# Kernel optimization log

Measured on AMD Instinct MI355X. Metric: run time of the kernel, lower is better.

## Reference

```python
import jax, jax.numpy as jnp
import numpy as np

EPS = 1e-5
NUM_PIXELS = 2  # M_Relax window half-width


def _conv(x, w, b, groups=1, pad=0):
    y = jax.lax.conv_general_dilated(
        x, w, (1, 1), [(pad, pad), (pad, pad)],
        dimension_numbers=("NCHW", "OIHW", "NCHW"),
        feature_group_count=groups)
    return y + b[None, :, None, None]


def _bn(x, g, bta, m, v):
    # eval-mode BatchNorm2d with running stats
    inv = jax.lax.rsqrt(v + EPS)
    return g[None, :, None, None] * (x - m[None, :, None, None]) * inv[None, :, None, None] + bta[None, :, None, None]


def _resb(x, w1, b1, w2, b2):
    y = _conv(x, w1, b1, groups=4, pad=1)
    y = jnp.where(y > 0, y, 0.1 * y)  # LeakyReLU(0.1)
    y = _conv(y, w2, b2, groups=4, pad=1)
    return y + x


def _relax(M):
    # M: (N, w, w); sum of shifts +-NUM_PIXELS along the row (dim 1)
    w = M.shape[1]
    P = jnp.pad(M, ((0, 0), (NUM_PIXELS, NUM_PIXELS), (0, 0)))
    out = P[:, 0:w, :]
    for k in range(1, 2 * NUM_PIXELS + 1):
        out = out + P[:, k:k + w, :]
    return out


def setup_inputs() -> dict:
    key = jax.random.key(0)
    ks = jax.random.split(key, 16)
    b, c, h, w = 4, 64, 128, 256
    c2 = 2 * c
    s = 0.05
    inp = {
        "x_left": jax.random.normal(ks[0], (b, c, h, w), jnp.float32),
        "x_right": jax.random.normal(ks[1], (b, c, h, w), jnp.float32),
        "conv1_w": jax.random.normal(ks[2], (c, c, 1, 1), jnp.float32) * s,
        "conv1_b": jnp.zeros((c,), jnp.float32),
        "conv2_w": jax.random.normal(ks[3], (c, c, 1, 1), jnp.float32) * s,
        "conv2_b": jnp.zeros((c,), jnp.float32),
        "bn_g": jnp.ones((c2,), jnp.float32),
        "bn_b": jnp.zeros((c2,), jnp.float32),
        "bn_m": jax.random.normal(ks[4], (c2,), jnp.float32) * 0.1,
        "bn_v": jax.random.uniform(ks[5], (c2,), jnp.float32) + 0.5,
        "rb_w1": jax.random.normal(ks[6], (c2, c2 // 4, 3, 3), jnp.float32) * s,
        "rb_b1": jnp.zeros((c2,), jnp.float32),
        "rb_w2": jax.random.normal(ks[7], (c2, c2 // 4, 3, 3), jnp.float32) * s,
        "rb_b2": jnp.zeros((c2,), jnp.float32),
        "bq_w": jax.random.normal(ks[8], (c, c, 1, 1), jnp.float32) * s,
        "bq_b": jnp.zeros((c,), jnp.float32),
        "bs_w": jax.random.normal(ks[9], (c, c, 1, 1), jnp.float32) * s,
        "bs_b": jnp.zeros((c,), jnp.float32),
    }
    return inp


def reference(x_left, x_right, conv1_w, conv1_b, conv2_w, conv2_b,
              bn_g, bn_b, bn_m, bn_v, rb_w1, rb_b1, rb_w2, rb_b2,
              bq_w, bq_b, bs_w, bs_b):
    b, c, h, w = x_left.shape
    cat_l = jnp.concatenate([_conv(x_left, conv1_w, conv1_b), x_left], axis=1)
    cat_r = jnp.concatenate([_conv(x_right, conv2_w, conv2_b), x_right], axis=1)
    Q = _conv(_resb(_bn(cat_l, bn_g, bn_b, bn_m, bn_v), rb_w1, rb_b1, rb_w2, rb_b2), bq_w, bq_b, groups=2)
    K = _conv(_resb(_bn(cat_r, bn_g, bn_b, bn_m, bn_v), rb_w1, rb_b1, rb_w2, rb_b2), bs_w, bs_b, groups=2)
    Q = Q - Q.mean(axis=3, keepdims=True)
    K = K - K.mean(axis=3, keepdims=True)
    # score: (b*h, w, w) -- per-epipolar-row cross-view attention
    Qr = Q.transpose(0, 2, 3, 1).reshape(b * h, w, c)
    Kr = K.transpose(0, 2, 1, 3).reshape(b * h, c, w)
    score = jnp.matmul(Qr, Kr)
    M_r2l = jax.nn.softmax(score, axis=-1)
    M_l2r = jax.nn.softmax(score.transpose(0, 2, 1), axis=-1)
    # validity maps via relaxed cycle-consistency (detached in original)
    V_l = jnp.einsum("nij,nji->ni", _relax(M_r2l), M_l2r)
    V_r = jnp.einsum("nij,nji->ni", _relax(M_l2r), M_r2l)
    V_l = jax.lax.stop_gradient(V_l).reshape(b, 1, h, w)
    V_r = jax.lax.stop_gradient(V_r).reshape(b, 1, h, w)
    V_l_t = jnp.tanh(5.0 * V_l)
    V_r_t = jnp.tanh(5.0 * V_r)
    xl = x_left.transpose(0, 2, 3, 1).reshape(b * h, w, c)
    xr = x_right.transpose(0, 2, 3, 1).reshape(b * h, w, c)
    x_lT = jnp.matmul(M_r2l, xr).reshape(b, h, w, c).transpose(0, 3, 1, 2)
    x_rT = jnp.matmul(M_l2r, xl).reshape(b, h, w, c).transpose(0, 3, 1, 2)
    out_left = x_left * (1.0 - V_l_t) + x_lT * V_l_t
    out_right = x_right * (1.0 - V_r_t) + x_rT * V_r_t
    return out_left, out_right
```

## Files before the change

### kernel.cpp

```cpp
#include <hip/hip_runtime.h>
#include <math.h>

#define BB 4
#define CC 64
#define C2 128
#define HH 128
#define WW 256
#define NN (BB*HH)
#define EPSBN 1e-5f

typedef _Float16 f16;
typedef _Float16 half8 __attribute__((ext_vector_type(8)));
typedef float f32x4 __attribute__((ext_vector_type(4)));

__global__ __launch_bounds__(256) void k_wprep(
    const float* __restrict__ w1, const float* __restrict__ w2,
    f16* __restrict__ wp1, f16* __restrict__ wp2)
{
    int g = blockIdx.x; int which = blockIdx.y;
    const float* src = which ? w2 : w1;
    f16* dst = which ? wp2 : wp1;
    for (int p = threadIdx.x; p < 9216; p += 256) {
        int mo = p / 288; int kr = p - mo*288;
        int ks = kr >> 5; int ic = kr & 31;
        dst[g*9216 + p] = (f16)src[((g*32 + mo)*32 + ic)*9 + ks];
    }
}

__global__ __launch_bounds__(256) void k_catbn_m(
    const float* __restrict__ x, const float* __restrict__ cw, const float* __restrict__ cb,
    const float* __restrict__ g, const float* __restrict__ bb_, const float* __restrict__ m,
    const float* __restrict__ v, f16* __restrict__ u)
{
    __shared__ f16 Xl[256][72];
    __shared__ f16 Wl[64][72];
    __shared__ float sS[64], sT[64], sS2[64], sT2[64];
    int n = blockIdx.x; int b = n >> 7; int h = n & 127; int t = threadIdx.x;
    for (int p = t; p < 2048; p += 256) {
        int idx = p * 2; int o = idx >> 6, i = idx & 63;
        union { f16 h[2]; unsigned int u1; } pr;
        pr.h[0] = (f16)cw[idx]; pr.h[1] = (f16)cw[idx + 1];
        *(unsigned int*)&Wl[o][i] = pr.u1;
    }
    if (t < 64) {
        float inv = rsqrtf(v[t] + EPSBN); float s = g[t] * inv;
        sS[t] = s; sT[t] = bb_[t] + s * (cb[t] - m[t]);
        float inv2 = rsqrtf(v[t + 64] + EPSBN); float s2 = g[t + 64] * inv2;
        sS2[t] = s2; sT2[t] = bb_[t + 64] - s2 * m[t + 64];
    }
    __syncthreads();
    f16* up = u + ((size_t)(n*256 + t)) * 128;
    for (int c8 = 0; c8 < 8; ++c8) {
        float xv8[8];
#pragma unroll
        for (int j = 0; j < 8; ++j)
            xv8[j] = x[(((b*64 + c8*8 + j)*128 + h) << 8) + t];
        union { f16 h[8]; uint4 v4; } pk;
#pragma unroll
        for (int j = 0; j < 8; ++j) {
            int c = c8*8 + j;
            pk.h[j] = (f16)(sS2[c]*xv8[j] + sT2[c]);
        }
        *(uint4*)(up + 64 + c8*8) = pk.v4;
#pragma unroll
        for (int j2 = 0; j2 < 4; ++j2) {
            union { f16 h[2]; unsigned int u1; } q;
            q.h[0] = (f16)xv8[j2*2]; q.h[1] = (f16)xv8[j2*2 + 1];
            *(unsigned int*)&Xl[t][c8*8 + j2*2] = q.u1;
        }
    }
    __syncthreads();
    int lane = t & 63, wv = t >> 6;
    int m16 = lane & 15, quad = lane >> 4;
    half8 af[4][2], bf[4][2];
#pragma unroll
    for (int mt = 0; mt < 4; ++mt)
#pragma unroll
        for (int kk = 0; kk < 2; ++kk)
            af[mt][kk] = *(const half8*)&Wl[mt*16 + m16][kk*32 + quad*8];
#pragma unroll
    for (int nt = 0; nt < 4; ++nt)
#pragma unroll
        for (int kk = 0; kk < 2; ++kk)
            bf[nt][kk] = *(const half8*)&Xl[wv*64 + nt*16 + m16][kk*32 + quad*8];
    f32x4 acc[4][4] = {};
#pragma unroll
    for (int mt = 0; mt < 4; ++mt)
#pragma unroll
        for (int nt = 0; nt < 4; ++nt) {
            acc[mt][nt] = __builtin_amdgcn_mfma_f32_16x16x32_f16(af[mt][0], bf[nt][0], acc[mt][nt], 0, 0, 0);
            acc[mt][nt] = __builtin_amdgcn_mfma_f32_16x16x32_f16(af[mt][1], bf[nt][1], acc[mt][nt], 0, 0, 0);
        }
#pragma unroll
    for (int mt = 0; mt < 4; ++mt) {
        int ocb = mt*16 + quad*4;
        float s4[4], t4[4];
        *(float4*)s4 = *(const float4*)&sS[ocb];
        *(float4*)t4 = *(const float4*)&sT[ocb];
#pragma unroll
        for (int nt = 0; nt < 4; ++nt) {
            int px = wv*64 + nt*16 + m16;
            union { f16 h[4]; uint2 u2; } ov;
#pragma unroll
            for (int r = 0; r < 4; ++r)
                ov.h[r] = (f16)(s4[r]*acc[mt][nt][r] + t4[r]);
            *(uint2*)(u + ((size_t)(n*256 + px))*128 + ocb) = ov.u2;
        }
    }
}

template<bool LEAKY, bool RES>
__global__ __launch_bounds__(256, 2) void k_conv3r(
    const f16* __restrict__ in, const f16* __restrict__ wp,
    const float* __restrict__ bias, const f16* __restrict__ res,
    f16* __restrict__ out)
{
    __shared__ f16 Xl[6*130*40];
    int b = blockIdx.x >> 5; int h0 = (blockIdx.x & 31) * 4;
    int g = blockIdx.y; int w0 = blockIdx.z * 128;
    int t = threadIdx.x;
    int lane = t & 63, wv = t >> 6;
    int m16 = lane & 15, quad = lane >> 4;
    const f16* wg = wp + g*9216;
    half8 af[2][9];
#pragma unroll
    for (int mt = 0; mt < 2; ++mt)
#pragma unroll
        for (int ks = 0; ks < 9; ++ks)
            af[mt][ks] = *(const half8*)(wg + (mt*16 + m16)*288 + ks*32 + quad*8);
    float bo[2][4];
#pragma unroll
    for (int mt = 0; mt < 2; ++mt)
#pragma unroll
        for (int r = 0; r < 4; ++r)
            bo[mt][r] = bias[g*32 + mt*16 + quad*4 + r];
    for (int idx = t; idx < 3120; idx += 256) {
        int r = idx / 520; int rem = idx - r*520; int p = rem >> 2; int q = rem & 3;
        int hr = h0 + r - 1; int wg2 = w0 + p - 1;
        uint4 val = make_uint4(0,0,0,0);
        if ((unsigned)wg2 < 256u && (unsigned)hr < 128u)
            val = *(const uint4*)(in + ((size_t)((b*128 + hr)*256 + wg2))*128 + g*32 + q*8);
        *(uint4*)&Xl[(r*130 + p)*40 + q*8] = val;
    }
    __syncthreads();
    int px0 = wv*32 + m16;
#pragma unroll
    for (int rr = 0; rr < 4; ++rr) {
        f32x4 acc[2][2] = {};
#pragma unroll
        for (int ks = 0; ks < 9; ++ks) {
            int ky = ks / 3, kx = ks - ky*3;
            half8 bf0 = *(const half8*)&Xl[((rr + ky)*130 + px0 + kx)*40 + quad*8];
            half8 bf1 = *(const half8*)&Xl[((rr + ky)*130 + px0 + 16 + kx)*40 + quad*8];
            acc[0][0] = __builtin_amdgcn_mfma_f32_16x16x32_f16(af[0][ks], bf0, acc[0][0], 0, 0, 0);
            acc[0][1] = __builtin_amdgcn_mfma_f32_16x16x32_f16(af[0][ks], bf1, acc[0][1], 0, 0, 0);
            acc[1][0] = __builtin_amdgcn_mfma_f32_16x16x32_f16(af[1][ks], bf0, acc[1][0], 0, 0, 0);
            acc[1][1] = __builtin_amdgcn_mfma_f32_16x16x32_f16(af[1][ks], bf1, acc[1][1], 0, 0, 0);
        }
        int h = h0 + rr;
#pragma unroll
        for (int mt = 0; mt < 2; ++mt)
#pragma unroll
            for (int nt = 0; nt < 2; ++nt) {
                int px = w0 + wv*32 + nt*16 + m16;
                int oc = g*32 + mt*16 + quad*4;
                size_t off = ((size_t)((b*128 + h)*256 + px))*128 + oc;
                float rv4[4] = {0.f, 0.f, 0.f, 0.f};
                if (RES) {
                    union { f16 h[4]; uint2 v2; } rrd;
                    rrd.v2 = *(const uint2*)(res + off);
#pragma unroll
                    for (int r = 0; r < 4; ++r) rv4[r] = (float)rrd.h[r];
                }
                union { f16 h[4]; uint2 v2; } ov;
#pragma unroll
                for (int r = 0; r < 4; ++r) {
                    float y = acc[mt][nt][r] + bo[mt][r];
                    if (LEAKY) y = y > 0.f ? y : 0.1f*y;
                    if (RES) y += rv4[r];
                    ov.h[r] = (f16)y;
                }
                *(uint2*)(out + off) = ov.v2;
            }
    }
}

__global__ __launch_bounds__(256, 2) void k_conv1x1m(
    const f16* __restrict__ in, const float* __restrict__ wgt,
    f16* __restrict__ outq)
{
    __shared__ f16 Xl[256][72];
    __shared__ f16 Wl[64][72];
    __shared__ float partial[4][64];
    __shared__ float meanS[64];
    int n = blockIdx.x; int t = threadIdx.x;
    int lane = t & 63, wv = t >> 6;
    int m16 = lane & 15, quad = lane >> 4;
    for (int p = t; p < 2048; p += 256) {
        int idx = p * 2; int o = idx >> 6, i = idx & 63;
        union { f16 h[2]; unsigned int u1; } pr;
        pr.h[0] = (f16)wgt[idx]; pr.h[1] = (f16)wgt[idx + 1];
        *(unsigned int*)&Wl[o][i] = pr.u1;
    }
    f32x4 acc[4][4] = {};
    const f16* rp = in + ((size_t)n*256 + t)*128;
    for (int g = 0; g < 2; ++g) {
#pragma unroll
        for (int i8 = 0; i8 < 8; ++i8)
            *(uint4*)&Xl[t][i8*8] = *(const uint4*)(rp + g*64 + i8*8);
        __syncthreads();
        half8 af[2][2], bf[4][2];
#pragma unroll
        for (int ml = 0; ml < 2; ++ml)
#pragma unroll
            for (int kk = 0; kk < 2; ++kk)
                af[ml][kk] = *(const half8*)&Wl[g*32 + ml*16 + m16][kk*32 + quad*8];
#pragma unroll
        for (int nt = 0; nt < 4; ++nt)
#pragma unroll
            for (int kk = 0; kk < 2; ++kk)
                bf[nt][kk] = *(const half8*)&Xl[wv*64 + nt*16 + m16][kk*32 + quad*8];
#pragma unroll
        for (int ml = 0; ml < 2; ++ml)
#pragma unroll
            for (int nt = 0; nt < 4; ++nt) {
                int mt = g*2 + ml;
                acc[mt][nt] = __builtin_amdgcn_mfma_f32_16x16x32_f16(af[ml][0], bf[nt][0], acc[mt][nt], 0, 0, 0);
                acc[mt][nt] = __builtin_amdgcn_mfma_f32_16x16x32_f16(af[ml][1], bf[nt][1], acc[mt][nt], 0, 0, 0);
            }
        __syncthreads();
    }
#pragma unroll
    for (int mt = 0; mt < 4; ++mt)
#pragma unroll
        for (int r = 0; r < 4; ++r) {
            float s = acc[mt][0][r] + acc[mt][1][r] + acc[mt][2][r] + acc[mt][3][r];
            s += __shfl_xor(s, 1); s += __shfl_xor(s, 2);
            s += __shfl_xor(s, 4); s += __shfl_xor(s, 8);
            if (m16 == 0) partial[wv][mt*16 + quad*4 + r] = s;
        }
    __syncthreads();
    if (t < 64)
        meanS[t] = (partial[0][t] + partial[1][t] + partial[2][t] + partial[3][t]) * (1.0f/256.0f);
    __syncthreads();
    f16* qp = outq + ((size_t)n*256)*64;
#pragma unroll
    for (int mt = 0; mt < 4; ++mt) {
        int ocb = mt*16 + quad*4;
        float m4[4]; *(float4*)m4 = *(const float4*)&meanS[ocb];
#pragma unroll
        for (int nt = 0; nt < 4; ++nt) {
            int px = wv*64 + nt*16 + m16;
            union { f16 h[4]; uint2 u2; } ov;
#pragma unroll
            for (int r = 0; r < 4; ++r)
                ov.h[r] = (f16)(acc[mt][nt][r] - m4[r]);
            *(uint2*)(qp + (size_t)px*64 + ocb) = ov.u2;
        }
    }
}

__global__ __launch_bounds__(512, 1) void k_attn(
    const f16* __restrict__ Aq, const f16* __restrict__ Bk,
    const float* __restrict__ xB, const float* __restrict__ xP,
    float* __restrict__ outp)
{
    __shared__ f16 Sl[65536];
    __shared__ f16 Pl[260][40];
    __shared__ f16 Xl[64][40];
    __shared__ float rmS[256], riS[256], cmS[256], ciS[256];
    __shared__ float scr[2][256];
    int n = blockIdx.x; int b = n >> 7; int h = n & 127;
    int t = threadIdx.x;
    int lane = t & 63, wv = t >> 6;
    int m16 = lane & 15, quad = lane >> 4;
    int W = wv * 32;

    const f16* ag = Aq + (size_t)n*16384;
    const f16* bg = Bk + (size_t)n*16384;
    half8 af1[2][2];
#pragma unroll
    for (int mt = 0; mt < 2; ++mt)
#pragma unroll
        for (int kk = 0; kk < 2; ++kk)
            af1[mt][kk] = *(const half8*)(ag + (size_t)(W + mt*16 + m16)*64 + kk*32 + quad*8);
    for (int jc = 0; jc < 256; jc += 64) {
        half8 bf1[4][2];
#pragma unroll
        for (int nt = 0; nt < 4; ++nt)
#pragma unroll
            for (int kk = 0; kk < 2; ++kk)
                bf1[nt][kk] = *(const half8*)(bg + (size_t)(jc + nt*16 + m16)*64 + kk*32 + quad*8);
        f32x4 acc1[2][4] = {};
#pragma unroll
        for (int mt = 0; mt < 2; ++mt)
#pragma unroll
            for (int nt = 0; nt < 4; ++nt) {
                acc1[mt][nt] = __builtin_amdgcn_mfma_f32_16x16x32_f16(af1[mt][0], bf1[nt][0], acc1[mt][nt], 0, 0, 0);
                acc1[mt][nt] = __builtin_amdgcn_mfma_f32_16x16x32_f16(af1[mt][1], bf1[nt][1], acc1[mt][nt], 0, 0, 0);
            }
#pragma unroll
        for (int mt = 0; mt < 2; ++mt)
#pragma unroll
            for (int nt = 0; nt < 4; ++nt)
#pragma unroll
                for (int r = 0; r < 4; ++r) {
                    int row = W + mt*16 + quad*4 + r;
                    int col = jc + nt*16 + m16;
                    int byte = (row << 9) + ((col*2) ^ ((row & 7) << 4));
                    *(f16*)((char*)Sl + byte) = (f16)acc1[mt][nt][r];
                }
    }
    __syncthreads();

    if (t < 256) {
        int r = t; int xo = (r & 7) << 4;
        const char* base = (const char*)Sl + (r << 9);
        float m = -1e30f;
#pragma unroll 4
        for (int g = 0; g < 32; ++g) {
            half8 v8 = *(const half8*)(base + ((g*16) ^ xo));
#pragma unroll
            for (int e = 0; e < 8; ++e) m = fmaxf(m, (float)v8[e]);
        }
        float s = 0.f;
#pragma unroll 4
        for (int g = 0; g < 32; ++g) {
            half8 v8 = *(const half8*)(base + ((g*16) ^ xo));
#pragma unroll
            for (int e = 0; e < 8; ++e) s += __expf((float)v8[e] - m);
        }
        rmS[r] = m; riS[r] = 1.0f/s;
    } else {
        int c = t - 256; int c2 = c*2;
        const char* base = (const char*)Sl;
        float m = -1e30f;
#pragma unroll 8
        for (int row = 0; row < 256; ++row) {
            f16 v = *(const f16*)(base + (row << 9) + (c2 ^ ((row & 7) << 4)));
            m = fmaxf(m, (float)v);
        }
        float s = 0.f;
#pragma unroll 8
        for (int row = 0; row < 256; ++row) {
            f16 v = *(const f16*)(base + (row << 9) + (c2 ^ ((row & 7) << 4)));
            s += __expf((float)v - m);
        }
        cmS[c] = m; ciS[c] = 1.0f/s;
    }
    if (t < 10)       *(uint4*)((char*)&Pl[0][0]   + t*16)      = make_uint4(0,0,0,0);
    else if (t < 20)  *(uint4*)((char*)&Pl[258][0] + (t-10)*16) = make_uint4(0,0,0,0);
    __syncthreads();

    int r = t & 255, hc = t >> 8;
    int cbase = hc * 16;
    float rm = rmS[r], ri = riS[r];
    int xc = t >> 3, xj = (t & 7) * 4;
    const float* xg = xB + ((size_t)(b*64 + xc)*128 + h)*256;
    f32x4 acc[2][4] = {};
    float vacc = 0.f;
    const char* sb = (const char*)Sl + (r << 9);
    int xo = (r & 7) << 4;
    for (int kc = 0; kc < 256; kc += 32) {
        float sraw[16];
        {
            half8 v0 = *(const half8*)(sb + ((((kc + cbase)*2))      ^ xo));
            half8 v1 = *(const half8*)(sb + ((((kc + cbase)*2) + 16) ^ xo));
            half8 p0, p1;
#pragma unroll
            for (int e = 0; e < 8; ++e) {
                sraw[e] = (float)v0[e];
                p0[e] = (f16)(__expf(sraw[e] - rm) * ri);
            }
#pragma unroll
            for (int e = 0; e < 8; ++e) {
                sraw[8 + e] = (float)v1[e];
                p1[e] = (f16)(__expf(sraw[8 + e] - rm) * ri);
            }
            char* pb = (char*)&Pl[r + 2][cbase];
            *(half8*)pb = p0; *(half8*)(pb + 16) = p1;
        }
        {
            float4 x4 = *(const float4*)(xg + kc + xj);
            union { f16 h[4]; uint2 v2; } px;
            px.h[0] = (f16)x4.x; px.h[1] = (f16)x4.y;
            px.h[2] = (f16)x4.z; px.h[3] = (f16)x4.w;
            *(uint2*)&Xl[xc][xj] = px.v2;
        }
        __syncthreads();
#pragma unroll
        for (int j8 = 0; j8 < 2; ++j8) {
            const char* wb = (const char*)&Pl[r][cbase + j8*8];
            half8 w0 = *(const half8*)(wb);
            half8 w1 = *(const half8*)(wb + 80);
            half8 w2 = *(const half8*)(wb + 160);
            half8 w3 = *(const half8*)(wb + 240);
            half8 w4 = *(const half8*)(wb + 320);
            half8 win = w0 + w1 + w2 + w3 + w4;
#pragma unroll
            for (int e = 0; e < 8; ++e) {
                int j = kc + cbase + j8*8 + e;
                float Bv = __expf(sraw[j8*8 + e] - cmS[j]) * ciS[j];
                vacc = fmaf((float)win[e], Bv, vacc);
            }
        }
        half8 pa[2], xb_[4];
#pragma unroll
        for (int mt = 0; mt < 2; ++mt)
            pa[mt] = *(const half8*)((const char*)&Pl[W + mt*16 + m16 + 2][0] + quad*16);
#pragma unroll
        for (int nt = 0; nt < 4; ++nt)
            xb_[nt] = *(const half8*)((const char*)&Xl[nt*16 + m16][0] + quad*16);
#pragma unroll
        for (int mt = 0; mt < 2; ++mt)
#pragma unroll
            for (int nt = 0; nt < 4; ++nt)
                acc[mt][nt] = __builtin_amdgcn_mfma_f32_16x16x32_f16(pa[mt], xb_[nt], acc[mt][nt], 0, 0, 0);
        __syncthreads();
    }
    scr[hc][r] = vacc;
    __syncthreads();
    if (t < 256) rmS[t] = scr[0][t] + scr[1][t];
    __syncthreads();
#pragma unroll
    for (int mt = 0; mt < 2; ++mt) {
        int i0 = W + mt*16 + quad*4;
        float v4[4];
        *(float4*)v4 = *(const float4*)&rmS[i0];
        float tv[4];
#pragma unroll
        for (int rr = 0; rr < 4; ++rr) tv[rr] = tanhf(5.f*v4[rr]);
#pragma unroll
        for (int nt = 0; nt < 4; ++nt) {
            int c = nt*16 + m16;
            size_t base = (((size_t)(b*64 + c)*128 + h) << 8) + i0;
            float xp4[4]; *(float4*)xp4 = *(const float4*)&xP[base];
            float o4[4];
#pragma unroll
            for (int rr = 0; rr < 4; ++rr)
                o4[rr] = xp4[rr]*(1.f - tv[rr]) + acc[mt][nt][rr]*tv[rr];
            *(float4*)&outp[base] = *(float4*)o4;
        }
    }
}

extern "C" void kernel_launch(void* const* d_in, const int* in_sizes, int n_in,
                              void* d_out, int out_size, void* d_ws, size_t ws_size,
                              hipStream_t stream)
{
    const float* x_left  = (const float*)d_in[0];
    const float* x_right = (const float*)d_in[1];
    const float* conv1_w = (const float*)d_in[2];
    const float* conv1_b = (const float*)d_in[3];
    const float* conv2_w = (const float*)d_in[4];
    const float* conv2_b = (const float*)d_in[5];
    const float* bn_g    = (const float*)d_in[6];
    const float* bn_b    = (const float*)d_in[7];
    const float* bn_m    = (const float*)d_in[8];
    const float* bn_v    = (const float*)d_in[9];
    const float* rb_w1   = (const float*)d_in[10];
    const float* rb_b1   = (const float*)d_in[11];
    const float* rb_w2   = (const float*)d_in[12];
    const float* rb_b2   = (const float*)d_in[13];
    const float* bq_w    = (const float*)d_in[14];
    const float* bs_w    = (const float*)d_in[16];

    f16* W16 = (f16*)d_ws;
    f16* u  = W16;
    f16* y1 = W16 + 16777216;
    f16* r  = W16 + 33554432;
    f16* Qh = W16 + 67108864;
    f16* Kh = W16 + 75497472;
    f16* Wp1 = W16 + 84934656;
    f16* Wp2 = W16 + 84971520;

    float* out_left  = (float*)d_out;
    float* out_right = (float*)d_out + 8388608;

    k_wprep<<<dim3(4, 2), 256, 0, stream>>>(rb_w1, rb_w2, Wp1, Wp2);

    k_catbn_m<<<NN, 256, 0, stream>>>(x_left, conv1_w, conv1_b, bn_g, bn_b, bn_m, bn_v, u);
    k_conv3r<true,  false><<<dim3(128, 4, 2), 256, 0, stream>>>(u, Wp1, rb_b1, nullptr, y1);
    k_conv3r<false, true ><<<dim3(128, 4, 2), 256, 0, stream>>>(y1, Wp2, rb_b2, u, r);
    k_conv1x1m<<<NN, 256, 0, stream>>>(r, bq_w, Qh);

    k_catbn_m<<<NN, 256, 0, stream>>>(x_right, conv2_w, conv2_b, bn_g, bn_b, bn_m, bn_v, u);
    k_conv3r<true,  false><<<dim3(128, 4, 2), 256, 0, stream>>>(u, Wp1, rb_b1, nullptr, y1);
    k_conv3r<false, true ><<<dim3(128, 4, 2), 256, 0, stream>>>(y1, Wp2, rb_b2, u, r);
    k_conv1x1m<<<NN, 256, 0, stream>>>(r, bs_w, Kh);

    k_attn<<<NN, 512, 0, stream>>>(Qh, Kh, x_right, x_left,  out_left);
    k_attn<<<NN, 512, 0, stream>>>(Kh, Qh, x_left,  x_right, out_right);
}
```

Measured before the change: 520.6 us.

## Fuse both attention directions into one kernel sharing score matrix and online softmax stats

Merges the two k_attn launches into a single kernel that computes the Q·K score tile once and reuses it transposed for the right-to-left pass. Row and column softmax max/sum are computed online from MFMA registers with wave shuffles instead of separate scans over shared memory. This removes a duplicate score GEMM and the serial column-reduction loop. The cost is strided transposed reads from shared memory in the second pass and more register pressure.

```diff
diff --git a/kernel.cpp b/kernel.cpp
--- a/kernel.cpp
+++ b/kernel.cpp
@@ -260,123 +260,51 @@
     }
 }
 
-__global__ __launch_bounds__(512, 1) void k_attn(
-    const f16* __restrict__ Aq, const f16* __restrict__ Bk,
+
+template<int RIGHT>
+__device__ __forceinline__ void attn_pass(
+    const char* Sl, char* pool,
+    const float* __restrict__ myM, const float* __restrict__ myI,
+    const float* __restrict__ oM,  const float* __restrict__ oI,
     const float* __restrict__ xB, const float* __restrict__ xP,
-    float* __restrict__ outp)
-{
-    __shared__ f16 Sl[65536];
-    __shared__ f16 Pl[260][40];
-    __shared__ f16 Xl[64][40];
-    __shared__ float rmS[256], riS[256], cmS[256], ciS[256];
-    __shared__ float scr[2][256];
-    int n = blockIdx.x; int b = n >> 7; int h = n & 127;
-    int t = threadIdx.x;
+    float* __restrict__ outp, int b, int h, int t)
+{
+    f16 (*Pl)[40] = (f16(*)[40])pool;
+    f16 (*Xl)[40] = (f16(*)[40])(pool + 20800);
+    float* scr = (float*)(pool + 20800);
+    float* Vv  = (float*)(pool + 22848);
     int lane = t & 63, wv = t >> 6;
     int m16 = lane & 15, quad = lane >> 4;
     int W = wv * 32;
-
-    const f16* ag = Aq + (size_t)n*16384;
-    const f16* bg = Bk + (size_t)n*16384;
-    half8 af1[2][2];
-#pragma unroll
-    for (int mt = 0; mt < 2; ++mt)
-#pragma unroll
-        for (int kk = 0; kk < 2; ++kk)
-            af1[mt][kk] = *(const half8*)(ag + (size_t)(W + mt*16 + m16)*64 + kk*32 + quad*8);
-    for (int jc = 0; jc < 256; jc += 64) {
-        half8 bf1[4][2];
-#pragma unroll
-        for (int nt = 0; nt < 4; ++nt)
-#pragma unroll
-            for (int kk = 0; kk < 2; ++kk)
-                bf1[nt][kk] = *(const half8*)(bg + (size_t)(jc + nt*16 + m16)*64 + kk*32 + quad*8);
-        f32x4 acc1[2][4] = {};
-#pragma unroll
-        for (int mt = 0; mt < 2; ++mt)
-#pragma unroll
-            for (int nt = 0; nt < 4; ++nt) {
-                acc1[mt][nt] = __builtin_amdgcn_mfma_f32_16x16x32_f16(af1[mt][0], bf1[nt][0], acc1[mt][nt], 0, 0, 0);
-                acc1[mt][nt] = __builtin_amdgcn_mfma_f32_16x16x32_f16(af1[mt][1], bf1[nt][1], acc1[mt][nt], 0, 0, 0);
-            }
-#pragma unroll
-        for (int mt = 0; mt < 2; ++mt)
-#pragma unroll
-            for (int nt = 0; nt < 4; ++nt)
-#pragma unroll
-                for (int r = 0; r < 4; ++r) {
-                    int row = W + mt*16 + quad*4 + r;
-                    int col = jc + nt*16 + m16;
-                    int byte = (row << 9) + ((col*2) ^ ((row & 7) << 4));
-                    *(f16*)((char*)Sl + byte) = (f16)acc1[mt][nt][r];
-                }
-    }
-    __syncthreads();
-
-    if (t < 256) {
-        int r = t; int xo = (r & 7) << 4;
-        const char* base = (const char*)Sl + (r << 9);
-        float m = -1e30f;
-#pragma unroll 4
-        for (int g = 0; g < 32; ++g) {
-            half8 v8 = *(const half8*)(base + ((g*16) ^ xo));
-#pragma unroll
-            for (int e = 0; e < 8; ++e) m = fmaxf(m, (float)v8[e]);
-        }
-        float s = 0.f;
-#pragma unroll 4
-        for (int g = 0; g < 32; ++g) {
-            half8 v8 = *(const half8*)(base + ((g*16) ^ xo));
-#pragma unroll
-            for (int e = 0; e < 8; ++e) s += __expf((float)v8[e] - m);
-        }
-        rmS[r] = m; riS[r] = 1.0f/s;
-    } else {
-        int c = t - 256; int c2 = c*2;
-        const char* base = (const char*)Sl;
-        float m = -1e30f;
-#pragma unroll 8
-        for (int row = 0; row < 256; ++row) {
-            f16 v = *(const f16*)(base + (row << 9) + (c2 ^ ((row & 7) << 4)));
-            m = fmaxf(m, (float)v);
-        }
-        float s = 0.f;
-#pragma unroll 8
-        for (int row = 0; row < 256; ++row) {
-            f16 v = *(const f16*)(base + (row << 9) + (c2 ^ ((row & 7) << 4)));
-            s += __expf((float)v - m);
-        }
-        cmS[c] = m; ciS[c] = 1.0f/s;
-    }
-    if (t < 10)       *(uint4*)((char*)&Pl[0][0]   + t*16)      = make_uint4(0,0,0,0);
-    else if (t < 20)  *(uint4*)((char*)&Pl[258][0] + (t-10)*16) = make_uint4(0,0,0,0);
-    __syncthreads();
-
     int r = t & 255, hc = t >> 8;
     int cbase = hc * 16;
-    float rm = rmS[r], ri = riS[r];
+    float rm = myM[r], ri = myI[r];
     int xc = t >> 3, xj = (t & 7) * 4;
     const float* xg = xB + ((size_t)(b*64 + xc)*128 + h)*256;
     f32x4 acc[2][4] = {};
     float vacc = 0.f;
-    const char* sb = (const char*)Sl + (r << 9);
+    const char* sb = Sl + (r << 9);
     int xo = (r & 7) << 4;
     for (int kc = 0; kc < 256; kc += 32) {
         float sraw[16];
+        if (!RIGHT) {
+            half8 v0 = *(const half8*)(sb + (((kc + cbase)*2)      ^ xo));
+            half8 v1 = *(const half8*)(sb + (((kc + cbase)*2 + 16) ^ xo));
+#pragma unroll
+            for (int e = 0; e < 8; ++e) { sraw[e] = (float)v0[e]; sraw[8+e] = (float)v1[e]; }
+        } else {
+#pragma unroll
+            for (int e = 0; e < 16; ++e) {
+                int j = kc + cbase + e;
+                sraw[e] = (float)*(const f16*)(Sl + (j << 9) + ((r*2) ^ ((j & 7) << 4)));
+            }
+        }
         {
-            half8 v0 = *(const half8*)(sb + ((((kc + cbase)*2))      ^ xo));
-            half8 v1 = *(const half8*)(sb + ((((kc + cbase)*2) + 16) ^ xo));
             half8 p0, p1;
 #pragma unroll
-            for (int e = 0; e < 8; ++e) {
-                sraw[e] = (float)v0[e];
-                p0[e] = (f16)(__expf(sraw[e] - rm) * ri);
-            }
-#pragma unroll
-            for (int e = 0; e < 8; ++e) {
-                sraw[8 + e] = (float)v1[e];
-                p1[e] = (f16)(__expf(sraw[8 + e] - rm) * ri);
-            }
+            for (int e = 0; e < 8; ++e) p0[e] = (f16)(__expf(sraw[e]     - rm) * ri);
+#pragma unroll
+            for (int e = 0; e < 8; ++e) p1[e] = (f16)(__expf(sraw[8 + e] - rm) * ri);
             char* pb = (char*)&Pl[r + 2][cbase];
             *(half8*)pb = p0; *(half8*)(pb + 16) = p1;
         }
@@ -400,7 +328,7 @@
 #pragma unroll
             for (int e = 0; e < 8; ++e) {
                 int j = kc + cbase + j8*8 + e;
-                float Bv = __expf(sraw[j8*8 + e] - cmS[j]) * ciS[j];
+                float Bv = __expf(sraw[j8*8 + e] - oM[j]) * oI[j];
                 vacc = fmaf((float)win[e], Bv, vacc);
             }
         }
@@ -418,15 +346,15 @@
                 acc[mt][nt] = __builtin_amdgcn_mfma_f32_16x16x32_f16(pa[mt], xb_[nt], acc[mt][nt], 0, 0, 0);
         __syncthreads();
     }
-    scr[hc][r] = vacc;
-    __syncthreads();
-    if (t < 256) rmS[t] = scr[0][t] + scr[1][t];
+    scr[hc*256 + r] = vacc;
+    __syncthreads();
+    if (t < 256) Vv[t] = scr[t] + scr[256 + t];
     __syncthreads();
 #pragma unroll
     for (int mt = 0; mt < 2; ++mt) {
         int i0 = W + mt*16 + quad*4;
         float v4[4];
-        *(float4*)v4 = *(const float4*)&rmS[i0];
+        *(float4*)v4 = *(const float4*)&Vv[i0];
         float tv[4];
 #pragma unroll
         for (int rr = 0; rr < 4; ++rr) tv[rr] = tanhf(5.f*v4[rr]);
@@ -442,6 +370,132 @@
             *(float4*)&outp[base] = *(float4*)o4;
         }
     }
+}
+
+__global__ __launch_bounds__(512, 1) void k_attn2(
+    const f16* __restrict__ Q, const f16* __restrict__ K,
+    const float* __restrict__ xl, const float* __restrict__ xr,
+    float* __restrict__ outL, float* __restrict__ outR)
+{
+    __shared__ f16 Sl[65536];
+    __shared__ __align__(16) char pool[25920];
+    __shared__ float rmS[256], riS[256], cmS[256], ciS[256];
+    float* colM = (float*)pool;
+    float* colS = (float*)(pool + 8192);
+    int n = blockIdx.x; int b = n >> 7; int h = n & 127;
+    int t = threadIdx.x;
+    int lane = t & 63, wv = t >> 6;
+    int m16 = lane & 15, quad = lane >> 4;
+    int W = wv * 32;
+
+    const f16* ag = Q + (size_t)n*16384;
+    const f16* bg = K + (size_t)n*16384;
+    half8 af1[2][2];
+#pragma unroll
+    for (int mt = 0; mt < 2; ++mt)
+#pragma unroll
+        for (int kk = 0; kk < 2; ++kk)
+            af1[mt][kk] = *(const half8*)(ag + (size_t)(W + mt*16 + m16)*64 + kk*32 + quad*8);
+    float rowm[8], rows_[8];
+#pragma unroll
+    for (int i = 0; i < 8; ++i) { rowm[i] = -1e30f; rows_[i] = 0.f; }
+    for (int jc = 0; jc < 256; jc += 64) {
+        half8 bf1[4][2];
+#pragma unroll
+        for (int nt = 0; nt < 4; ++nt)
+#pragma unroll
+            for (int kk = 0; kk < 2; ++kk)
+                bf1[nt][kk] = *(const half8*)(bg + (size_t)(jc + nt*16 + m16)*64 + kk*32 + quad*8);
+        f32x4 acc1[2][4] = {};
+#pragma unroll
+        for (int mt = 0; mt < 2; ++mt)
+#pragma unroll
+            for (int nt = 0; nt < 4; ++nt) {
+                acc1[mt][nt] = __builtin_amdgcn_mfma_f32_16x16x32_f16(af1[mt][0], bf1[nt][0], acc1[mt][nt], 0, 0, 0);
+                acc1[mt][nt] = __builtin_amdgcn_mfma_f32_16x16x32_f16(af1[mt][1], bf1[nt][1], acc1[mt][nt], 0, 0, 0);
+            }
+#pragma unroll
+        for (int mt = 0; mt < 2; ++mt)
+#pragma unroll
+            for (int nt = 0; nt < 4; ++nt)
+#pragma unroll
+                for (int r = 0; r < 4; ++r) {
+                    int row = W + mt*16 + quad*4 + r;
+                    int col = jc + nt*16 + m16;
+                    f16 hv = (f16)acc1[mt][nt][r];
+                    *(f16*)((char*)Sl + (row << 9) + ((col*2) ^ ((row & 7) << 4))) = hv;
+                    acc1[mt][nt][r] = (float)hv;
+                }
+#pragma unroll
+        for (int mt = 0; mt < 2; ++mt)
+#pragma unroll
+            for (int r = 0; r < 4; ++r) {
+                float lm = fmaxf(fmaxf(acc1[mt][0][r], acc1[mt][1][r]),
+                                 fmaxf(acc1[mt][2][r], acc1[mt][3][r]));
+                lm = fmaxf(lm, __shfl_xor(lm, 1));
+                lm = fmaxf(lm, __shfl_xor(lm, 2));
+                lm = fmaxf(lm, __shfl_xor(lm, 4));
+                lm = fmaxf(lm, __shfl_xor(lm, 8));
+                float le = __expf(acc1[mt][0][r] - lm) + __expf(acc1[mt][1][r] - lm)
+                         + __expf(acc1[mt][2][r] - lm) + __expf(acc1[mt][3][r] - lm);
+                le += __shfl_xor(le, 1); le += __shfl_xor(le, 2);
+                le += __shfl_xor(le, 4); le += __shfl_xor(le, 8);
+                int idx = mt*4 + r;
+                float nm = fmaxf(rowm[idx], lm);
+                rows_[idx] = rows_[idx]*__expf(rowm[idx] - nm) + le*__expf(lm - nm);
+                rowm[idx] = nm;
+            }
+#pragma unroll
+        for (int nt = 0; nt < 4; ++nt) {
+            float lm = acc1[0][nt][0];
+#pragma unroll
+            for (int r = 1; r < 4; ++r) lm = fmaxf(lm, acc1[0][nt][r]);
+#pragma unroll
+            for (int r = 0; r < 4; ++r) lm = fmaxf(lm, acc1[1][nt][r]);
+            lm = fmaxf(lm, __shfl_xor(lm, 16));
+            lm = fmaxf(lm, __shfl_xor(lm, 32));
+            float le = 0.f;
+#pragma unroll
+            for (int mt2 = 0; mt2 < 2; ++mt2)
+#pragma unroll
+                for (int r = 0; r < 4; ++r) le += __expf(acc1[mt2][nt][r] - lm);
+            le += __shfl_xor(le, 16); le += __shfl_xor(le, 32);
+            if (quad == 0) {
+                int col = jc + nt*16 + m16;
+                colM[wv*256 + col] = lm;
+                colS[wv*256 + col] = le;
+            }
+        }
+    }
+    if (m16 == 0) {
+#pragma unroll
+        for (int mt = 0; mt < 2; ++mt)
+#pragma unroll
+            for (int r = 0; r < 4; ++r) {
+                int row = W + mt*16 + quad*4 + r;
+                rmS[row] = rowm[mt*4 + r];
+                riS[row] = 1.0f / rows_[mt*4 + r];
+            }
+    }
+    __syncthreads();
+    if (t < 256) {
+        float m = colM[t], s = colS[t];
+#pragma unroll
+        for (int w = 1; w < 8; ++w) {
+            float m2 = colM[w*256 + t], s2 = colS[w*256 + t];
+            float nm = fmaxf(m, m2);
+            s = s*__expf(m - nm) + s2*__expf(m2 - nm);
+            m = nm;
+        }
+        cmS[t] = m; ciS[t] = 1.0f / s;
+    }
+    __syncthreads();
+    if (t < 10)       *(uint4*)(pool + t*16)           = make_uint4(0,0,0,0);
+    else if (t < 20)  *(uint4*)(pool + 20640 + (t-10)*16) = make_uint4(0,0,0,0);
+
+    attn_pass<0>((const char*)Sl, pool, rmS, riS, cmS, ciS, xr, xl, outL, b, h, t);
+    __syncthreads();
+    attn_pass<1>((const char*)Sl, pool, cmS, ciS, rmS, riS, xl, xr, outR, b, h, t);
 }
 
 extern "C" void kernel_launch(void* const* d_in, const int* in_sizes, int n_in,
@@ -489,6 +543,5 @@
     k_conv3r<false, true ><<<dim3(128, 4, 2), 256, 0, stream>>>(y1, Wp2, rb_b2, u, r);
     k_conv1x1m<<<NN, 256, 0, stream>>>(r, bs_w, Kh);
 
-    k_attn<<<NN, 512, 0, stream>>>(Qh, Kh, x_right, x_left,  out_left);
-    k_attn<<<NN, 512, 0, stream>>>(Kh, Qh, x_left,  x_right, out_right);
-}
+    k_attn2<<<NN, 512, 0, stream>>>(Qh, Kh, x_left, x_right, out_left, out_right);
+}
```

Result: faster. 438.3 us (-15.8%).
